# Performance work log

Hardware: AMD Instinct MI355X
Metric: run time of the kernel (lower is better)

Reference implementation:

```python
import jax, jax.numpy as jnp
import numpy as np

B, T, D = 2, 2048, 2048
H = 8
DK = 256   # head_qk_dim
DV = 512   # head_v_dim
C = 64     # retention chunk size
EPS = 1e-5
ROPE_BASE = 10000.0


def _rotary(x):
    # x: [B, T, H, DK], non-interleaved (rotate-half) rotary over full head dim
    half = DK // 2
    inv_freq = 1.0 / (ROPE_BASE ** (jnp.arange(0, DK, 2, dtype=jnp.float32) / DK))
    freqs = jnp.arange(T, dtype=jnp.float32)[:, None] * inv_freq[None, :]  # [T, half]
    cos = jnp.cos(freqs)[None, :, None, :].astype(x.dtype)
    sin = jnp.sin(freqs)[None, :, None, :].astype(x.dtype)
    x1, x2 = x[..., :half], x[..., half:]
    return jnp.concatenate([x1 * cos - x2 * sin, x2 * cos + x1 * sin], axis=-1)


def setup_inputs() -> dict:
    key = jax.random.key(0)
    ks = jax.random.split(key, 6)
    s = 2.0 ** (-2.5) * (2.0 / 2048.0) ** 0.5  # xavier_uniform-ish scale, gain 2^-2.5
    return {
        "hidden_states": jax.random.normal(ks[0], (B, T, D), jnp.float32),
        "Wq": jax.random.normal(ks[1], (H * DK, D), jnp.float32) * s,
        "Wk": jax.random.normal(ks[2], (H * DK, D), jnp.float32) * s,
        "Wv": jax.random.normal(ks[3], (H * DV, D), jnp.float32) * s,
        "Wg": jax.random.normal(ks[4], (H * DV, D), jnp.float32) * s,
        "Wo": jax.random.normal(ks[5], (D, H * DV), jnp.float32) * s,
        "g_norm_weight": jnp.ones((DV,), jnp.float32),
    }


def reference(hidden_states, Wq, Wk, Wv, Wg, Wo, g_norm_weight):
    x = hidden_states  # [B, T, D]
    q = (x @ Wq.T).reshape(B, T, H, DK)
    k = (x @ Wk.T).reshape(B, T, H, DK)
    q = _rotary(q)
    k = _rotary(k)
    q = q.transpose(0, 2, 1, 3) * (DK ** -0.5)        # [B, H, T, DK]
    k = k.transpose(0, 2, 1, 3)                       # [B, H, T, DK]
    v = (x @ Wv.T).reshape(B, T, H, DV).transpose(0, 2, 1, 3)  # [B, H, T, DV]

    # RetNet multi-scale per-head decay
    logb = jnp.log(1.0 - 2.0 ** (-5.0 - jnp.arange(H, dtype=jnp.float32)))  # [H]
    i = jnp.arange(C, dtype=jnp.float32)
    # intra-chunk decay mask b^{i-j} for i>=j: [H, C, C]
    Dmask = jnp.where(i[:, None] >= i[None, :],
                      jnp.exp(logb[:, None, None] * (i[:, None] - i[None, :])), 0.0)
    q_dec = jnp.exp(logb[:, None] * (i + 1.0))        # [H, C]  decay applied to q vs carried state
    k_dec = jnp.exp(logb[:, None] * (C - 1.0 - i))    # [H, C]  decay applied to k for state update
    chunk_dec = jnp.exp(logb * C)                     # [H]

    N = T // C
    qc = q.reshape(B, H, N, C, DK).transpose(2, 0, 1, 3, 4)  # [N, B, H, C, DK]
    kc = k.reshape(B, H, N, C, DK).transpose(2, 0, 1, 3, 4)
    vc = v.reshape(B, H, N, C, DV).transpose(2, 0, 1, 3, 4)

    def body(S, inp):
        qi, ki, vi = inp  # [B,H,C,DK], [B,H,C,DK], [B,H,C,DV]
        inter = jnp.einsum('bhcd,bhdv->bhcv', qi * q_dec[None, :, :, None], S)
        scores = jnp.einsum('bhcd,bhmd->bhcm', qi, ki) * Dmask[None]
        o = inter + jnp.einsum('bhcm,bhmv->bhcv', scores, vi)
        S_new = S * chunk_dec[None, :, None, None] + \
                jnp.einsum('bhcd,bhcv->bhdv', ki * k_dec[None, :, :, None], vi)
        return S_new, o

    S0 = jnp.zeros((B, H, DK, DV), x.dtype)
    _, oc = jax.lax.scan(body, S0, (qc, kc, vc))  # oc: [N, B, H, C, DV]
    o = oc.transpose(1, 2, 0, 3, 4).reshape(B, H, T, DV).transpose(0, 2, 1, 3)  # [B, T, H, DV]

    g = (x @ Wg.T).reshape(B, T, H, DV)
    # fused RMSNorm + swish gate (per head_v_dim)
    o_n = o * jax.lax.rsqrt(jnp.mean(o * o, axis=-1, keepdims=True) + EPS) * g_norm_weight
    o = o_n * (g * jax.nn.sigmoid(g))
    return o.reshape(B, T, H * DV) @ Wo.T  # [B, T, D]
```

## Files before the change

### kernel.cpp

```cpp
#include <hip/hip_runtime.h>


typedef unsigned short u16;
typedef unsigned int u32;
typedef short bf16x8 __attribute__((ext_vector_type(8)));
typedef short s16x4 __attribute__((ext_vector_type(4)));
typedef float f32x4 __attribute__((ext_vector_type(4)));
typedef u32 u32x2 __attribute__((ext_vector_type(2)));
typedef u32 u32x4 __attribute__((ext_vector_type(4)));

typedef __attribute__((address_space(3))) u32 lds_u32;
typedef __attribute__((address_space(1))) const u32 gbl_u32;

__device__ __forceinline__ float bf2f(u16 u) {
    union { u32 i; float f; } x; x.i = ((u32)u) << 16; return x.f;
}
__device__ __forceinline__ u16 f2bf(float f) {
    union { float f; u32 i; } x; x.f = f;
    u32 u = x.i;
    u += 0x7fffu + ((u >> 16) & 1u);
    return (u16)(u >> 16);
}
__device__ __forceinline__ f32x4 mfma16(bf16x8 a, bf16x8 b, f32x4 c) {
    return __builtin_amdgcn_mfma_f32_16x16x32_bf16(a, b, c, 0, 0, 0);
}
__device__ __forceinline__ void gload16(const u16* g, u16* lds) {
    __builtin_amdgcn_global_load_lds((gbl_u32*)(unsigned long long)g,
                                     (lds_u32*)(u32)(unsigned long long)lds, 16, 0, 0);
}

__global__ __launch_bounds__(256)
void cvt_bf16(const float* __restrict__ src, u16* __restrict__ dst)
{
    size_t i = ((size_t)blockIdx.x * 256 + threadIdx.x) * 8;
    f32x4 a = *(const f32x4*)(src + i);
    f32x4 b = *(const f32x4*)(src + i + 4);
    bf16x8 r;
#pragma unroll
    for (int j = 0; j < 4; j++) { r[j] = (short)f2bf(a[j]); r[j + 4] = (short)f2bf(b[j]); }
    *(bf16x8*)(dst + i) = r;
}

template<bool CF32>
__global__ __launch_bounds__(256, 2)
void gemm_bt(const u16* __restrict__ A, const u16* __restrict__ Bm,
             void* __restrict__ Cv, int N, int K)
{
    __shared__ u16 Ab[128 * 64];
    __shared__ u16 Bb[128 * 64];
    const int tid = threadIdx.x;
    const int lane = tid & 63, wave = tid >> 6;
    const int quad = lane >> 4, l16 = lane & 15;
    const int tn = blockIdx.x, tm = blockIdx.y;
    const int wr = wave >> 1, wc = wave & 1;

    f32x4 acc[4][4];
#pragma unroll
    for (int i = 0; i < 4; i++)
#pragma unroll
        for (int j = 0; j < 4; j++) acc[i][j] = (f32x4){0.f, 0.f, 0.f, 0.f};

    const u16* Abase = A + (size_t)tm * 128 * K;
    const u16* Bbase = Bm + (size_t)tn * 128 * K;
    const int rsub = lane >> 3, csub = (lane & 7) * 8;

    for (int k0 = 0; k0 < K; k0 += 64) {
        __syncthreads();
#pragma unroll
        for (int i = 0; i < 4; i++) {
            int chunk = wave * 4 + i;
            int r = chunk * 8 + rsub;
            gload16(Abase + (size_t)r * K + k0 + csub, Ab + chunk * 512);
            gload16(Bbase + (size_t)r * K + k0 + csub, Bb + chunk * 512);
        }
        __syncthreads();
#pragma unroll
        for (int kc = 0; kc < 2; kc++) {
            bf16x8 af[4], bfr[4];
#pragma unroll
            for (int mt = 0; mt < 4; mt++)
                af[mt] = *(const bf16x8*)(Ab + (wr * 64 + mt * 16 + l16) * 64 + kc * 32 + quad * 8);
#pragma unroll
            for (int nt = 0; nt < 4; nt++)
                bfr[nt] = *(const bf16x8*)(Bb + (wc * 64 + nt * 16 + l16) * 64 + kc * 32 + quad * 8);
#pragma unroll
            for (int mt = 0; mt < 4; mt++)
#pragma unroll
                for (int nt = 0; nt < 4; nt++)
                    acc[mt][nt] = mfma16(af[mt], bfr[nt], acc[mt][nt]);
        }
    }
    const int row0 = tm * 128 + wr * 64 + quad * 4;
    const int col0 = tn * 128 + wc * 64 + l16;
#pragma unroll
    for (int mt = 0; mt < 4; mt++)
#pragma unroll
        for (int nt = 0; nt < 4; nt++)
#pragma unroll
            for (int r = 0; r < 4; r++) {
                size_t idx = (size_t)(row0 + mt * 16 + r) * N + col0 + nt * 16;
                if constexpr (CF32) ((float*)Cv)[idx] = acc[mt][nt][r];
                else                ((u16*)Cv)[idx]   = f2bf(acc[mt][nt][r]);
            }
}

__global__ __launch_bounds__(512, 2)
void gemm256(const u16* __restrict__ A, const u16* __restrict__ Bm,
             u16* __restrict__ C, int N, int K)
{
    __shared__ __align__(16) u16 As[2][2][256 * 32];
    __shared__ __align__(16) u16 Bs[2][2][256 * 32];
    const int tid = threadIdx.x;
    const int lane = tid & 63, wave = tid >> 6;
    const int quad = lane >> 4, l16 = lane & 15;
    const int wm = wave >> 2, wn = wave & 3;
    const int tn = blockIdx.x, tm = blockIdx.y;
    const int NTm1 = K / 64 - 1;
    const u16* Abase = A + (size_t)tm * 256 * K;
    const u16* Bbase = Bm + (size_t)tn * 256 * K;
    const int gr = tid >> 2;
    const int gc = (tid & 3) * 8;
    const int wv64 = wave * 64;

    f32x4 acc[8][4];
#pragma unroll
    for (int i = 0; i < 8; i++)
#pragma unroll
        for (int j = 0; j < 4; j++) acc[i][j] = (f32x4){0.f, 0.f, 0.f, 0.f};

    bf16x8 bq[8];
    bf16x8 af[4];

#define STAGE(arr, bf, kc, Gb, kt) do {                                         \
    int kt_ = (kt); kt_ = (kt_ > NTm1) ? NTm1 : kt_;                            \
    const u16* s_ = (Gb) + (size_t)gr * K + (size_t)kt_ * 64 + (kc) * 32 + gc;  \
    gload16(s_,                 &arr[bf][kc][wv64 * 8]);                        \
    gload16(s_ + (size_t)128 * K, &arr[bf][kc][(512 + wv64) * 8]);              \
} while (0)

#define LDA(bf, kc, mg) do {                                                    \
    _Pragma("unroll")                                                           \
    for (int j = 0; j < 4; j++)                                                 \
        af[j] = *(const bf16x8*)&As[bf][kc][(wm * 128 + (mg) * 64 + j * 16 + l16) * 32 + quad * 8]; \
} while (0)

#define LDB(bf) do {                                                            \
    _Pragma("unroll")                                                           \
    for (int kc_ = 0; kc_ < 2; kc_++)                                           \
        _Pragma("unroll")                                                       \
        for (int n_ = 0; n_ < 4; n_++)                                          \
            bq[kc_ * 4 + n_] = *(const bf16x8*)&Bs[bf][kc_][(wn * 64 + n_ * 16 + l16) * 32 + quad * 8]; \
} while (0)

#define MM16(kc, mg) do {                                                       \
    _Pragma("unroll")                                                           \
    for (int j = 0; j < 4; j++)                                                 \
        _Pragma("unroll")                                                       \
        for (int n_ = 0; n_ < 4; n_++)                                          \
            acc[(mg) * 4 + j][n_] = mfma16(af[j], bq[(kc) * 4 + n_], acc[(mg) * 4 + j][n_]); \
} while (0)

#define BAR   __builtin_amdgcn_s_barrier()
#define LGKM0 asm volatile("s_waitcnt lgkmcnt(0)" ::: "memory")
#define VM6   asm volatile("s_waitcnt vmcnt(6)" ::: "memory")
#define PRIO1 __builtin_amdgcn_s_setprio(1)
#define PRIO0 __builtin_amdgcn_s_setprio(0)

    STAGE(Bs, 0, 0, Bbase, 0);
    STAGE(Bs, 0, 1, Bbase, 0);
    STAGE(As, 0, 0, Abase, 0);
    STAGE(As, 0, 1, Abase, 0);
    asm volatile("s_waitcnt vmcnt(4)" ::: "memory");
    STAGE(Bs, 1, 0, Bbase, 1);
    STAGE(Bs, 1, 1, Bbase, 1);
    STAGE(As, 1, 0, Abase, 1);
    asm volatile("s_waitcnt vmcnt(6)" ::: "memory");
    BAR;

    const int NI = K / 128;
    for (int it = 0; it < NI; ++it) {
        const int t0 = 2 * it;
        LDB(0); LDA(0, 0, 0); STAGE(As, 1, 1, Abase, t0 + 1);
        BAR; LGKM0; PRIO1; MM16(0, 0); PRIO0; BAR;
        LDA(0, 0, 1); STAGE(Bs, 0, 0, Bbase, t0 + 2);
        BAR; LGKM0; PRIO1; MM16(0, 1); PRIO0; BAR;
        LDA(0, 1, 0); STAGE(Bs, 0, 1, Bbase, t0 + 2);
        BAR; LGKM0; PRIO1; MM16(1, 0); PRIO0; BAR;
        LDA(0, 1, 1); STAGE(As, 0, 0, Abase, t0 + 2);
        BAR; LGKM0; PRIO1; MM16(1, 1); PRIO0; VM6; BAR;
        LDB(1); LDA(1, 0, 0); STAGE(As, 0, 1, Abase, t0 + 2);
        BAR; LGKM0; PRIO1; MM16(0, 0); PRIO0; BAR;
        LDA(1, 0, 1); STAGE(Bs, 1, 0, Bbase, t0 + 3);
        BAR; LGKM0; PRIO1; MM16(0, 1); PRIO0; BAR;
        LDA(1, 1, 0); STAGE(Bs, 1, 1, Bbase, t0 + 3);
        BAR; LGKM0; PRIO1; MM16(1, 0); PRIO0; BAR;
        LDA(1, 1, 1); STAGE(As, 1, 0, Abase, t0 + 3);
        BAR; LGKM0; PRIO1; MM16(1, 1); PRIO0; VM6; BAR;
    }
    asm volatile("s_waitcnt vmcnt(0)" ::: "memory");

    const int row0 = tm * 256 + wm * 128 + quad * 4;
    const int col0 = tn * 256 + wn * 64 + l16;
#pragma unroll
    for (int mt = 0; mt < 8; mt++)
#pragma unroll
        for (int nt = 0; nt < 4; nt++)
#pragma unroll
            for (int r = 0; r < 4; r++)
                C[(size_t)(row0 + mt * 16 + r) * N + col0 + nt * 16] = f2bf(acc[mt][nt][r]);

#undef STAGE
#undef LDA
#undef LDB
#undef MM16
#undef BAR
#undef LGKM0
#undef VM6
#undef PRIO1
#undef PRIO0
}

__global__ __launch_bounds__(256, 2)
void rotary_scores(u16* __restrict__ q, const u16* __restrict__ k,
                   u16* __restrict__ kT, u16* __restrict__ P)
{
    __shared__ u16 qS[64 * 264];
    __shared__ u16 kS[64 * 264];
    const int tid = threadIdx.x;
    const int lane = tid & 63, wave = tid >> 6;
    const int quad = lane >> 4, l16 = lane & 15;
    const int bx = blockIdx.x;
    const int bh = bx & 15, n = bx >> 4;
    const int b = bh >> 3, h = bh & 7;
    const int t0 = n * 64;

    const int row = tid >> 2;
    const int j0 = (tid & 3) * 32;
    const size_t rowbase = (size_t)(b * 2048 + t0 + row) * 4096 + h * 256;
    const float tpos = (float)(t0 + row);
#pragma unroll
    for (int i = 0; i < 4; i++) {
        int j = j0 + i * 8;
        bf16x8 x1 = *(const bf16x8*)(q + rowbase + j);
        bf16x8 x2 = *(const bf16x8*)(q + rowbase + j + 128);
        bf16x8 y1 = *(const bf16x8*)(k + rowbase + j);
        bf16x8 y2 = *(const bf16x8*)(k + rowbase + j + 128);
        bf16x8 o1, o2, p1, p2;
#pragma unroll
        for (int e = 0; e < 8; e++) {
            float inv = expf((-9.210340371976184f / 128.f) * (float)(j + e));
            float ang = tpos * inv;
            float sv = sinf(ang), cv = cosf(ang);
            float a = bf2f((u16)x1[e]), bb = bf2f((u16)x2[e]);
            o1[e] = (short)f2bf((a * cv - bb * sv) * 0.0625f);
            o2[e] = (short)f2bf((bb * cv + a * sv) * 0.0625f);
            float e1 = bf2f((u16)y1[e]), e2 = bf2f((u16)y2[e]);
            p1[e] = (short)f2bf(e1 * cv - e2 * sv);
            p2[e] = (short)f2bf(e2 * cv + e1 * sv);
        }
        *(bf16x8*)(q + rowbase + j)       = o1;
        *(bf16x8*)(q + rowbase + j + 128) = o2;
        *(bf16x8*)(qS + row * 264 + j)       = o1;
        *(bf16x8*)(qS + row * 264 + j + 128) = o2;
        *(bf16x8*)(kS + row * 264 + j)       = p1;
        *(bf16x8*)(kS + row * 264 + j + 128) = p2;
    }
    __syncthreads();

    const float logb = logf(1.0f - exp2f(-5.0f - (float)h));
    f32x4 sc[4];
#pragma unroll
    for (int i = 0; i < 4; i++) sc[i] = (f32x4){0.f, 0.f, 0.f, 0.f};
#pragma unroll
    for (int kc = 0; kc < 8; kc++) {
        bf16x8 af = *(const bf16x8*)(qS + (wave * 16 + l16) * 264 + kc * 32 + quad * 8);
#pragma unroll
        for (int mt = 0; mt < 4; mt++) {
            bf16x8 bk = *(const bf16x8*)(kS + (mt * 16 + l16) * 264 + kc * 32 + quad * 8);
            sc[mt] = mfma16(af, bk, sc[mt]);
        }
    }
    u16* Pb = P + ((size_t)(bh * 32 + n)) * 64 * 64;
#pragma unroll
    for (int r = 0; r < 4; r++) {
        int cr = wave * 16 + quad * 4 + r;
        float rowe = __expf(logb * (float)(cr - 63));
#pragma unroll
        for (int mt = 0; mt < 4; mt++) {
            int m = mt * 16 + l16;
            float val = (cr >= m) ? sc[mt][r] * rowe : 0.0f;
            Pb[cr * 64 + m] = f2bf(val);
        }
    }

    const int d = tid;
    u16* dst = kT + ((size_t)(bh * 256 + d)) * 2048 + t0;
#pragma unroll
    for (int g8 = 0; g8 < 8; g8++) {
        bf16x8 w;
#pragma unroll
        for (int e = 0; e < 8; e++) w[e] = (short)kS[(g8 * 8 + e) * 264 + d];
        *(bf16x8*)(dst + g8 * 8) = w;
    }
}

__global__ __launch_bounds__(512, 2)
void retention(const u16* __restrict__ Q, const u16* __restrict__ KT,
               const u16* __restrict__ V, const u16* __restrict__ P,
               u16* __restrict__ O)
{
    __shared__ u16 St[32 * 264];
    __shared__ u16 vsT[32 * 72];

    const int tid = threadIdx.x;
    const int lane = tid & 63, wave = tid >> 6;
    const int quad = lane >> 4, l16 = lane & 15;
    const int bx = blockIdx.x;
    const int bh = bx & 15, vt = bx >> 4;
    const int b = bh >> 3, h = bh & 7;
    const int cgrp = wave >> 1, vhalf = wave & 1;

    const float logb = logf(1.0f - exp2f(-5.0f - (float)h));
    const float cdec = __expf(logb * 64.0f);

    int cr[4];
    float qdecr[4];
#pragma unroll
    for (int r = 0; r < 4; r++) {
        cr[r] = cgrp * 16 + quad * 4 + r;
        qdecr[r] = __expf(logb * (float)(cr[r] + 1));
    }
    const int mv = tid >> 3;
    const int vc4 = (tid & 7) * 4;
    const float kdv = __expf(logb * (float)(63 - mv));

    for (int i = tid; i < 32 * 264; i += 512) St[i] = 0;

    f32x4 Sacc[2][2];
#pragma unroll
    for (int dt = 0; dt < 2; dt++)
#pragma unroll
        for (int nt = 0; nt < 2; nt++) Sacc[dt][nt] = (f32x4){0.f, 0.f, 0.f, 0.f};

    for (int n = 0; n < 32; n++) {
        const int t0 = n * 64;
        u32x2 vv = *(const u32x2*)(V + (size_t)(b * 2048 + t0 + mv) * 4096 + h * 512 + vt * 32 + vc4);
        bf16x8 qf[8];
#pragma unroll
        for (int kc = 0; kc < 8; kc++)
            qf[kc] = *(const bf16x8*)(Q + (size_t)(b * 2048 + t0 + cgrp * 16 + l16) * 4096
                                      + h * 256 + kc * 32 + quad * 8);
        bf16x8 ktf[2][2];
#pragma unroll
        for (int dt = 0; dt < 2; dt++)
#pragma unroll
            for (int kc2 = 0; kc2 < 2; kc2++)
                ktf[dt][kc2] = *(const bf16x8*)(KT + (size_t)(bh * 256 + wave * 32 + dt * 16 + l16) * 2048
                                                + t0 + kc2 * 32 + quad * 8);
        bf16x8 pf[2];
#pragma unroll
        for (int kc2 = 0; kc2 < 2; kc2++)
            pf[kc2] = *(const bf16x8*)(P + ((size_t)(bh * 32 + n) * 64 + cgrp * 16 + l16) * 64
                                       + kc2 * 32 + quad * 8);

        __syncthreads();

        {
            u16 e0 = (u16)(vv[0] & 0xffff), e1 = (u16)(vv[0] >> 16);
            u16 e2 = (u16)(vv[1] & 0xffff), e3 = (u16)(vv[1] >> 16);
            vsT[(vc4 + 0) * 72 + mv] = f2bf(bf2f(e0) * kdv);
            vsT[(vc4 + 1) * 72 + mv] = f2bf(bf2f(e1) * kdv);
            vsT[(vc4 + 2) * 72 + mv] = f2bf(bf2f(e2) * kdv);
            vsT[(vc4 + 3) * 72 + mv] = f2bf(bf2f(e3) * kdv);
        }
        f32x4 oacc = (f32x4){0.f, 0.f, 0.f, 0.f};
#pragma unroll
        for (int kc = 0; kc < 8; kc++) {
            bf16x8 bs = *(const bf16x8*)(St + (vhalf * 16 + l16) * 264 + kc * 32 + quad * 8);
            oacc = mfma16(qf[kc], bs, oacc);
        }

        __syncthreads();

#pragma unroll
        for (int dt = 0; dt < 2; dt++)
#pragma unroll
            for (int nt = 0; nt < 2; nt++)
#pragma unroll
                for (int e = 0; e < 4; e++) Sacc[dt][nt][e] *= cdec;
#pragma unroll
        for (int kc2 = 0; kc2 < 2; kc2++) {
            bf16x8 bv0 = *(const bf16x8*)(vsT + l16 * 72 + kc2 * 32 + quad * 8);
            bf16x8 bv1 = *(const bf16x8*)(vsT + (16 + l16) * 72 + kc2 * 32 + quad * 8);
#pragma unroll
            for (int dt = 0; dt < 2; dt++) {
                Sacc[dt][0] = mfma16(ktf[dt][kc2], bv0, Sacc[dt][0]);
                Sacc[dt][1] = mfma16(ktf[dt][kc2], bv1, Sacc[dt][1]);
            }
        }
#pragma unroll
        for (int r = 0; r < 4; r++) oacc[r] *= qdecr[r];
#pragma unroll
        for (int kc2 = 0; kc2 < 2; kc2++) {
            bf16x8 bv = *(const bf16x8*)(vsT + (vhalf * 16 + l16) * 72 + kc2 * 32 + quad * 8);
            oacc = mfma16(pf[kc2], bv, oacc);
        }
#pragma unroll
        for (int r = 0; r < 4; r++)
            O[(size_t)(b * 2048 + t0 + cr[r]) * 4096 + h * 512 + vt * 32 + vhalf * 16 + l16] =
                f2bf(oacc[r]);
#pragma unroll
        for (int dt = 0; dt < 2; dt++)
#pragma unroll
            for (int nt = 0; nt < 2; nt++) {
                s16x4 w;
#pragma unroll
                for (int r = 0; r < 4; r++) w[r] = (short)f2bf(Sacc[dt][nt][r]);
                *(s16x4*)(St + (nt * 16 + l16) * 264 + wave * 32 + dt * 16 + quad * 4) = w;
            }
    }
}

__global__ __launch_bounds__(256)
void norm_gate(const u16* __restrict__ O, const u16* __restrict__ G,
               const float* __restrict__ gw, u16* __restrict__ ON)
{
    const int lane = threadIdx.x & 63;
    const size_t row = (size_t)blockIdx.x * 4 + (threadIdx.x >> 6);
    bf16x8 ov = *(const bf16x8*)(O + row * 512 + lane * 8);
    bf16x8 gv = *(const bf16x8*)(G + row * 512 + lane * 8);
    f32x4 w0 = *(const f32x4*)(gw + lane * 8);
    f32x4 w1 = *(const f32x4*)(gw + lane * 8 + 4);
    float of[8], gf[8];
    float ss = 0.f;
#pragma unroll
    for (int j = 0; j < 8; j++) {
        of[j] = bf2f((u16)ov[j]);
        gf[j] = bf2f((u16)gv[j]);
        ss += of[j] * of[j];
    }
#pragma unroll
    for (int off = 32; off > 0; off >>= 1) ss += __shfl_down(ss, off);
    ss = __shfl(ss, 0);
    const float rms = rsqrtf(ss * (1.0f / 512.0f) + 1e-5f);
    bf16x8 res;
#pragma unroll
    for (int j = 0; j < 8; j++) {
        float wj = (j < 4) ? w0[j] : w1[j - 4];
        float xn = of[j] * rms * wj;
        float sg = gf[j] / (1.f + __expf(-gf[j]));
        res[j] = (short)f2bf(xn * sg);
    }
    *(bf16x8*)(ON + row * 512 + lane * 8) = res;
}

extern "C" void kernel_launch(void* const* d_in, const int* in_sizes, int n_in,
                              void* d_out, int out_size, void* d_ws, size_t ws_size,
                              hipStream_t stream)
{
    const float* x  = (const float*)d_in[0];
    const float* Wq = (const float*)d_in[1];
    const float* Wk = (const float*)d_in[2];
    const float* Wv = (const float*)d_in[3];
    const float* Wg = (const float*)d_in[4];
    const float* Wo = (const float*)d_in[5];
    const float* gw = (const float*)d_in[6];
    float* out = (float*)d_out;

    const size_t M8 = (size_t)4096 * 2048;
    u16* Pb = (u16*)d_ws;
    u16* qk = Pb + (size_t)16 * 32 * 64 * 64;
    u16* kT = qk + 2 * M8;
    u16* v  = kT + M8;
    u16* o  = v + 2 * M8;
    u16* xb = o + 2 * M8;
    u16* g  = qk;
    u16* on = v;
    u16* wt = kT;

    dim3 blk(256, 1, 1), blk512(512, 1, 1);
    cvt_bf16<<<dim3(4096, 1, 1), blk, 0, stream>>>(x, xb);

    cvt_bf16<<<dim3(2048, 1, 1), blk, 0, stream>>>(Wq, wt);
    cvt_bf16<<<dim3(2048, 1, 1), blk, 0, stream>>>(Wk, wt + (size_t)2048 * 2048);
    gemm256<<<dim3(16, 16, 1), blk512, 0, stream>>>(xb, wt, qk, 4096, 2048);
    cvt_bf16<<<dim3(4096, 1, 1), blk, 0, stream>>>(Wv, wt);
    gemm256<<<dim3(16, 16, 1), blk512, 0, stream>>>(xb, wt, v, 4096, 2048);

    rotary_scores<<<dim3(512, 1, 1), blk, 0, stream>>>(qk, qk + 2048, kT, Pb);
    retention<<<dim3(256, 1, 1), blk512, 0, stream>>>(qk, kT, v, Pb, o);

    cvt_bf16<<<dim3(4096, 1, 1), blk, 0, stream>>>(Wg, kT);
    gemm256<<<dim3(16, 16, 1), blk512, 0, stream>>>(xb, kT, g, 4096, 2048);
    norm_gate<<<dim3(8192, 1, 1), blk, 0, stream>>>(o, g, gw, on);
    cvt_bf16<<<dim3(4096, 1, 1), blk, 0, stream>>>(Wo, kT);
    gemm_bt<true><<<dim3(16, 32, 1), blk, 0, stream>>>(on, kT, out, 2048, 4096);
}
```

Measured before the change: 621.1 us.

## Double-buffer retention state and V tiles, prefetch next chunk into registers

The retention kernel now keeps two LDS copies of the carried state and of the decayed V tile, so each chunk needs one barrier instead of two. Global loads of Q, K^T and P for the next chunk, and of V two chunks ahead, are issued into alternating register sets before the current chunk's work. The goal is to hide global load latency behind the current chunk's MFMA work and to cut barrier stalls in the sequential scan. In exchange it doubles the operand registers and the LDS footprint. Under the 512-thread, 2-blocks launch bounds this may cause spills or lower occupancy.

```diff
diff --git a/kernel.cpp b/kernel.cpp
--- a/kernel.cpp
+++ b/kernel.cpp
@@ -309,8 +309,8 @@
                const u16* __restrict__ V, const u16* __restrict__ P,
                u16* __restrict__ O)
 {
-    __shared__ u16 St[32 * 264];
-    __shared__ u16 vsT[32 * 72];
+    __shared__ u16 St[2][32 * 264];
+    __shared__ u16 vsT[2][32 * 72];
 
     const int tid = threadIdx.x;
     const int lane = tid & 63, wave = tid >> 6;
@@ -334,7 +334,12 @@
     const int vc4 = (tid & 7) * 4;
     const float kdv = __expf(logb * (float)(63 - mv));
 
-    for (int i = tid; i < 32 * 264; i += 512) St[i] = 0;
+    for (int i = tid; i < 32 * 264; i += 512) { St[0][i] = 0; St[1][i] = 0; }
+
+    const u16* Qp  = Q  + (size_t)(b * 2048 + cgrp * 16 + l16) * 4096 + h * 256 + quad * 8;
+    const u16* KTp = KT + (size_t)(bh * 256 + wave * 32 + l16) * 2048 + quad * 8;
+    const u16* Pp  = P  + ((size_t)(bh * 32) * 64 + cgrp * 16 + l16) * 64 + quad * 8;
+    const u16* Vp  = V  + (size_t)(b * 2048 + mv) * 4096 + h * 512 + vt * 32 + vc4;
 
     f32x4 Sacc[2][2];
 #pragma unroll
@@ -342,83 +347,110 @@
 #pragma unroll
         for (int nt = 0; nt < 2; nt++) Sacc[dt][nt] = (f32x4){0.f, 0.f, 0.f, 0.f};
 
-    for (int n = 0; n < 32; n++) {
-        const int t0 = n * 64;
-        u32x2 vv = *(const u32x2*)(V + (size_t)(b * 2048 + t0 + mv) * 4096 + h * 512 + vt * 32 + vc4);
-        bf16x8 qf[8];
-#pragma unroll
-        for (int kc = 0; kc < 8; kc++)
-            qf[kc] = *(const bf16x8*)(Q + (size_t)(b * 2048 + t0 + cgrp * 16 + l16) * 4096
-                                      + h * 256 + kc * 32 + quad * 8);
-        bf16x8 ktf[2][2];
-#pragma unroll
-        for (int dt = 0; dt < 2; dt++)
-#pragma unroll
-            for (int kc2 = 0; kc2 < 2; kc2++)
-                ktf[dt][kc2] = *(const bf16x8*)(KT + (size_t)(bh * 256 + wave * 32 + dt * 16 + l16) * 2048
-                                                + t0 + kc2 * 32 + quad * 8);
-        bf16x8 pf[2];
-#pragma unroll
-        for (int kc2 = 0; kc2 < 2; kc2++)
-            pf[kc2] = *(const bf16x8*)(P + ((size_t)(bh * 32 + n) * 64 + cgrp * 16 + l16) * 64
-                                       + kc2 * 32 + quad * 8);
-
-        __syncthreads();
-
-        {
-            u16 e0 = (u16)(vv[0] & 0xffff), e1 = (u16)(vv[0] >> 16);
-            u16 e2 = (u16)(vv[1] & 0xffff), e3 = (u16)(vv[1] >> 16);
-            vsT[(vc4 + 0) * 72 + mv] = f2bf(bf2f(e0) * kdv);
-            vsT[(vc4 + 1) * 72 + mv] = f2bf(bf2f(e1) * kdv);
-            vsT[(vc4 + 2) * 72 + mv] = f2bf(bf2f(e2) * kdv);
-            vsT[(vc4 + 3) * 72 + mv] = f2bf(bf2f(e3) * kdv);
-        }
-        f32x4 oacc = (f32x4){0.f, 0.f, 0.f, 0.f};
-#pragma unroll
-        for (int kc = 0; kc < 8; kc++) {
-            bf16x8 bs = *(const bf16x8*)(St + (vhalf * 16 + l16) * 264 + kc * 32 + quad * 8);
-            oacc = mfma16(qf[kc], bs, oacc);
-        }
-
-        __syncthreads();
-
-#pragma unroll
-        for (int dt = 0; dt < 2; dt++)
-#pragma unroll
-            for (int nt = 0; nt < 2; nt++)
-#pragma unroll
-                for (int e = 0; e < 4; e++) Sacc[dt][nt][e] *= cdec;
-#pragma unroll
-        for (int kc2 = 0; kc2 < 2; kc2++) {
-            bf16x8 bv0 = *(const bf16x8*)(vsT + l16 * 72 + kc2 * 32 + quad * 8);
-            bf16x8 bv1 = *(const bf16x8*)(vsT + (16 + l16) * 72 + kc2 * 32 + quad * 8);
-#pragma unroll
-            for (int dt = 0; dt < 2; dt++) {
-                Sacc[dt][0] = mfma16(ktf[dt][kc2], bv0, Sacc[dt][0]);
-                Sacc[dt][1] = mfma16(ktf[dt][kc2], bv1, Sacc[dt][1]);
-            }
-        }
-#pragma unroll
-        for (int r = 0; r < 4; r++) oacc[r] *= qdecr[r];
-#pragma unroll
-        for (int kc2 = 0; kc2 < 2; kc2++) {
-            bf16x8 bv = *(const bf16x8*)(vsT + (vhalf * 16 + l16) * 72 + kc2 * 32 + quad * 8);
-            oacc = mfma16(pf[kc2], bv, oacc);
-        }
-#pragma unroll
-        for (int r = 0; r < 4; r++)
-            O[(size_t)(b * 2048 + t0 + cr[r]) * 4096 + h * 512 + vt * 32 + vhalf * 16 + l16] =
-                f2bf(oacc[r]);
-#pragma unroll
-        for (int dt = 0; dt < 2; dt++)
-#pragma unroll
-            for (int nt = 0; nt < 2; nt++) {
-                s16x4 w;
-#pragma unroll
-                for (int r = 0; r < 4; r++) w[r] = (short)f2bf(Sacc[dt][nt][r]);
-                *(s16x4*)(St + (nt * 16 + l16) * 264 + wave * 32 + dt * 16 + quad * 4) = w;
-            }
-    }
+    bf16x8 qfA[8], qfB[8], ktA[4], ktB[4], pfA[2], pfB[2];
+    u32x2 vvA, vvB;
+
+#define LOADSET(nn, qf, kt, pf, vvn, nv) do {                                   \
+    const int nL = (nn), vL = (nv);                                             \
+    _Pragma("unroll")                                                           \
+    for (int kc = 0; kc < 8; kc++)                                              \
+        qf[kc] = *(const bf16x8*)(Qp + (size_t)nL * (64 * 4096) + kc * 32);     \
+    _Pragma("unroll")                                                           \
+    for (int dt = 0; dt < 2; dt++)                                              \
+        _Pragma("unroll")                                                       \
+        for (int kc2 = 0; kc2 < 2; kc2++)                                       \
+            kt[dt * 2 + kc2] = *(const bf16x8*)(KTp + dt * (16 * 2048) + nL * 64 + kc2 * 32); \
+    _Pragma("unroll")                                                           \
+    for (int kc2 = 0; kc2 < 2; kc2++)                                           \
+        pf[kc2] = *(const bf16x8*)(Pp + (size_t)nL * (64 * 64) + kc2 * 32);     \
+    vvn = *(const u32x2*)(Vp + (size_t)vL * (64 * 4096));                       \
+} while (0)
+
+    u32x2 vv0 = *(const u32x2*)(Vp);
+    LOADSET(0, qfA, ktA, pfA, vvA, 1);
+    {
+        u16 e0 = (u16)(vv0[0] & 0xffff), e1 = (u16)(vv0[0] >> 16);
+        u16 e2 = (u16)(vv0[1] & 0xffff), e3 = (u16)(vv0[1] >> 16);
+        vsT[0][(vc4 + 0) * 72 + mv] = f2bf(bf2f(e0) * kdv);
+        vsT[0][(vc4 + 1) * 72 + mv] = f2bf(bf2f(e1) * kdv);
+        vsT[0][(vc4 + 2) * 72 + mv] = f2bf(bf2f(e2) * kdv);
+        vsT[0][(vc4 + 3) * 72 + mv] = f2bf(bf2f(e3) * kdv);
+    }
+
+#define CHUNK(nn, qfC, ktC, pfC, vvC, qfN, ktN, pfN, vvN) do {                  \
+    const int nC = (nn);                                                        \
+    const int nP = (nC + 1 < 32) ? nC + 1 : 31;                                 \
+    const int nV = (nC + 2 < 32) ? nC + 2 : 31;                                 \
+    LOADSET(nP, qfN, ktN, pfN, vvN, nV);         \
+    asm volatile("s_waitcnt lgkmcnt(0)" ::: "memory");                          \
+    __builtin_amdgcn_s_barrier();                                               \
+    __builtin_amdgcn_sched_barrier(0);                                          \
+    {                                 \
+        u16* vd = &vsT[(nC + 1) & 1][0];                                        \
+        u16 e0 = (u16)(vvC[0] & 0xffff), e1 = (u16)(vvC[0] >> 16);              \
+        u16 e2 = (u16)(vvC[1] & 0xffff), e3 = (u16)(vvC[1] >> 16);              \
+        vd[(vc4 + 0) * 72 + mv] = f2bf(bf2f(e0) * kdv);                         \
+        vd[(vc4 + 1) * 72 + mv] = f2bf(bf2f(e1) * kdv);                         \
+        vd[(vc4 + 2) * 72 + mv] = f2bf(bf2f(e2) * kdv);                         \
+        vd[(vc4 + 3) * 72 + mv] = f2bf(bf2f(e3) * kdv);                         \
+    }                                                                           \
+                        \
+    f32x4 oacc = (f32x4){0.f, 0.f, 0.f, 0.f};                                   \
+    _Pragma("unroll")                                                           \
+    for (int kc = 0; kc < 8; kc++) {                                            \
+        bf16x8 bs = *(const bf16x8*)(&St[(nC + 1) & 1][0]                       \
+                     + (vhalf * 16 + l16) * 264 + kc * 32 + quad * 8);          \
+        oacc = mfma16(qfC[kc], bs, oacc);                                       \
+    }                                                                           \
+                        \
+    _Pragma("unroll")                                                           \
+    for (int dt = 0; dt < 2; dt++)                                              \
+        _Pragma("unroll")                                                       \
+        for (int nt = 0; nt < 2; nt++)                                          \
+            _Pragma("unroll")                                                   \
+            for (int e = 0; e < 4; e++) Sacc[dt][nt][e] *= cdec;                \
+    _Pragma("unroll")                                                           \
+    for (int kc2 = 0; kc2 < 2; kc2++) {                                         \
+        bf16x8 bv0 = *(const bf16x8*)(&vsT[nC & 1][0] + l16 * 72 + kc2 * 32 + quad * 8);        \
+        bf16x8 bv1 = *(const bf16x8*)(&vsT[nC & 1][0] + (16 + l16) * 72 + kc2 * 32 + quad * 8); \
+        _Pragma("unroll")                                                       \
+        for (int dt = 0; dt < 2; dt++) {                                        \
+            Sacc[dt][0] = mfma16(ktC[dt * 2 + kc2], bv0, Sacc[dt][0]);          \
+            Sacc[dt][1] = mfma16(ktC[dt * 2 + kc2], bv1, Sacc[dt][1]);          \
+        }                                                                       \
+    }                                                                           \
+                                              \
+    _Pragma("unroll")                                                           \
+    for (int r = 0; r < 4; r++) oacc[r] *= qdecr[r];                            \
+    _Pragma("unroll")                                                           \
+    for (int kc2 = 0; kc2 < 2; kc2++) {                                         \
+        bf16x8 bv = *(const bf16x8*)(&vsT[nC & 1][0]                            \
+                     + (vhalf * 16 + l16) * 72 + kc2 * 32 + quad * 8);          \
+        oacc = mfma16(pfC[kc2], bv, oacc);                                      \
+    }                                                                           \
+    _Pragma("unroll")                                                           \
+    for (int r = 0; r < 4; r++)                                                 \
+        O[(size_t)(b * 2048 + nC * 64 + cr[r]) * 4096 + h * 512 + vt * 32       \
+          + vhalf * 16 + l16] = f2bf(oacc[r]);                                  \
+                                       \
+    _Pragma("unroll")                                                           \
+    for (int dt = 0; dt < 2; dt++)                                              \
+        _Pragma("unroll")                                                       \
+        for (int nt = 0; nt < 2; nt++) {                                        \
+            s16x4 w;                                                            \
+            _Pragma("unroll")                                                   \
+            for (int r = 0; r < 4; r++) w[r] = (short)f2bf(Sacc[dt][nt][r]);    \
+            *(s16x4*)(&St[nC & 1][0] + (nt * 16 + l16) * 264 + wave * 32        \
+                      + dt * 16 + quad * 4) = w;                                \
+        }                                                                       \
+} while (0)
+
+    for (int m = 0; m < 16; m++) {
+        CHUNK(2 * m,     qfA, ktA, pfA, vvA, qfB, ktB, pfB, vvB);
+        CHUNK(2 * m + 1, qfB, ktB, pfB, vvB, qfA, ktA, pfA, vvA);
+    }
+#undef CHUNK
+#undef LOADSET
 }
 
 __global__ __launch_bounds__(256)
```

Result: faster. 601.8 us (-3.1%).
